# Kernel optimization log

Measured on AMD Instinct MI355X. Metric: run time of the kernel, lower is better.

The kernel has to match this reference:

```python
import jax, jax.numpy as jnp
import numpy as np

MARGIN = 1.0


def setup_inputs() -> dict:
    key = jax.random.key(0)
    k1, k2 = jax.random.split(key)
    N, D = 8192, 128
    embeddings = jax.random.normal(k1, (N, D), dtype=jnp.float32)
    labels = jax.random.randint(k2, (N,), 0, 100, dtype=jnp.int64)
    return {"embeddings": embeddings, "labels": labels}


def reference(embeddings, labels):
    N = embeddings.shape[0]
    # Pairwise Euclidean distances (torch.cdist p=2) via the expanded form.
    sq = jnp.sum(embeddings * embeddings, axis=-1)  # [N]
    d2 = sq[:, None] + sq[None, :] - 2.0 * (embeddings @ embeddings.T)  # [N, N]
    d2 = jnp.maximum(d2, 0.0)
    eye = jnp.eye(N, dtype=bool)
    # Diagonal distances are never used (masked out below); replace the zero
    # under the sqrt to keep gradients finite.
    dist = jnp.sqrt(jnp.where(eye, 1.0, d2))  # [N, N]

    same = labels[:, None] == labels[None, :]
    pos_mask = same & ~eye
    neg_mask = (~same) & ~eye

    # sum_exp_i depends only on row i: one masked row reduction, reused for all pairs.
    sum_exp = jnp.sum(jnp.where(neg_mask, jnp.exp(MARGIN - dist), 0.0), axis=1)  # [N]

    # L_ij = log(sum_exp_i + sum_exp_j) + d_ij, only on positive pairs.
    L = jnp.log(sum_exp[:, None] + sum_exp[None, :]) + dist  # [N, N]
    per_pair = jnp.where(pos_mask, jax.nn.relu(L) ** 2, 0.0)
    n_pos = jnp.sum(pos_mask).astype(per_pair.dtype)
    return jnp.sum(per_pair) / n_pos / 2.0
```

## Files before the change

### kernel.cpp

```cpp
#include <hip/hip_runtime.h>
#include <hip/hip_bf16.h>


typedef __attribute__((ext_vector_type(8))) short bf16x8;
typedef __attribute__((ext_vector_type(4))) float f32x4;

__device__ __forceinline__ unsigned short f2bf(float f) {
    unsigned u = __float_as_uint(f);
    u += 0x7fffu + ((u >> 16) & 1u);
    return (unsigned short)(u >> 16);
}

__global__ __launch_bounds__(256) void setup_kernel(
    const float* __restrict__ e, const int* __restrict__ labels,
    float* __restrict__ sq, unsigned* __restrict__ ebf,
    float* __restrict__ sum_exp,
    int* __restrict__ counts_out, int* __restrict__ offsets_out,
    int* __restrict__ idxbuf, unsigned* __restrict__ ticket, int N)
{
    const int tid = threadIdx.x;
    if ((int)blockIdx.x < (int)gridDim.x - 1) {
        const int lane = tid & 63, wid = tid >> 6;
        if (tid < 32) sum_exp[blockIdx.x * 32 + tid] = 0.f;
        const int rowbase = (blockIdx.x * 4 + wid) * 8;
        #pragma unroll
        for (int it = 0; it < 8; ++it) {
            int row = rowbase + it;
            if (row >= N) break;
            float2 v = ((const float2*)(e + (size_t)row * 128))[lane];
            float s = v.x * v.x + v.y * v.y;
            #pragma unroll
            for (int off = 1; off < 64; off <<= 1) s += __shfl_xor(s, off, 64);
            if (lane == 0) sq[row] = s;
            unsigned bits = (unsigned)f2bf(v.x) | ((unsigned)f2bf(v.y) << 16);
            ebf[(size_t)row * 64 + lane] = bits;
        }
    } else {
        __shared__ int cnt[256];
        __shared__ int off[256];
        if (tid == 0) *ticket = 0u;
        cnt[tid] = 0;
        __syncthreads();
        for (int i = tid; i < N; i += 256)
            atomicAdd(&cnt[(unsigned)labels[i] & 255u], 1);
        __syncthreads();
        if (tid < 64) {
            int base = tid * 4;
            int c0 = cnt[base], c1 = cnt[base+1], c2 = cnt[base+2], c3 = cnt[base+3];
            int s = c0 + c1 + c2 + c3;
            int v = s;
            #pragma unroll
            for (int d = 1; d < 64; d <<= 1) {
                int u = __shfl_up(v, d, 64);
                if (tid >= d) v += u;
            }
            int excl = v - s;
            off[base]     = excl;
            off[base + 1] = excl + c0;
            off[base + 2] = excl + c0 + c1;
            off[base + 3] = excl + c0 + c1 + c2;
        }
        __syncthreads();
        counts_out[tid]  = cnt[tid];
        offsets_out[tid] = off[tid];
        cnt[tid] = off[tid];
        __syncthreads();
        for (int i = tid; i < N; i += 256) {
            int l = (unsigned)labels[i] & 255u;
            int p = atomicAdd(&cnt[l], 1);
            idxbuf[p] = i;
        }
    }
}

__global__ __launch_bounds__(512) void pass1_kernel(
    const unsigned short* __restrict__ ebf,
    const float* __restrict__ sq,
    const int* __restrict__ labels,
    float* __restrict__ sum_exp,
    int N, int nCb)
{
    __shared__ __align__(16) char a_tile[128 * 128];
    __shared__ __align__(16) char b_tile[128 * 128];
    __shared__ float rowsum[128];
    __shared__ float colsum[128];

    const int tid = threadIdx.x;
    const int lane = tid & 63, wid = tid >> 6;

    const int t = blockIdx.x;
    int bi = (int)((2.f * nCb + 1.f - __builtin_amdgcn_sqrtf(
                   (2.f * nCb + 1.f) * (2.f * nCb + 1.f) - 8.f * t)) * 0.5f);
    if (bi < 0) bi = 0;
    if (bi > nCb - 1) bi = nCb - 1;
    while (bi + 1 <= nCb - 1 && (bi + 1) * (2 * nCb - bi) / 2 <= t) ++bi;
    while (bi > 0 && bi * (2 * nCb - bi + 1) / 2 > t) --bi;
    const int bj = bi + (t - bi * (2 * nCb - bi + 1) / 2);
    const bool diag = (bi == bj);
    const int brow = bi * 128, bcol = bj * 128;

    if (tid < 128) { rowsum[tid] = 0.f; colsum[tid] = 0.f; }

    const int wm = (wid >> 2) * 64, wn = (wid & 3) * 32;
    const int lhi = lane >> 4, llo = lane & 15;
    const char* ebfB = (const char*)ebf;

    f32x4 acc[4][2];
    #pragma unroll
    for (int m = 0; m < 4; ++m)
        #pragma unroll
        for (int n = 0; n < 2; ++n)
            acc[m][n] = (f32x4){0.f, 0.f, 0.f, 0.f};

    #pragma unroll
    for (int c = 0; c < 2; ++c) {
        #pragma unroll
        for (int k = 0; k < 4; ++k) {
            int s = wid * 256 + k * 64;
            int tsel = s >> 10;
            int ls = s & 1023;
            int sl = ls + lane;
            int r = sl >> 3, j = sl & 7;
            int grow = (tsel ? bcol : brow) + r;
            const void* g = ebfB + ((size_t)grow << 8) + c * 128 + ((j ^ (r & 7)) << 4);
            char* l = (tsel ? b_tile : a_tile) + ls * 16;
            __builtin_amdgcn_global_load_lds(
                (const __attribute__((address_space(1))) unsigned*)g,
                (__attribute__((address_space(3))) unsigned*)l, 16, 0, 0);
        }
        __syncthreads();

        #pragma unroll
        for (int h = 0; h < 2; ++h) {
            const int cb = h * 64 + lhi * 16;
            bf16x8 af[4], bfr[2];
            #pragma unroll
            for (int m = 0; m < 4; ++m) {
                int r = wm + m * 16 + llo;
                af[m] = *(const bf16x8*)(a_tile + r * 128 + (cb ^ ((r & 7) << 4)));
            }
            #pragma unroll
            for (int n = 0; n < 2; ++n) {
                int r = wn + n * 16 + llo;
                bfr[n] = *(const bf16x8*)(b_tile + r * 128 + (cb ^ ((r & 7) << 4)));
            }
            #pragma unroll
            for (int m = 0; m < 4; ++m)
                #pragma unroll
                for (int n = 0; n < 2; ++n)
                    acc[m][n] = __builtin_amdgcn_mfma_f32_16x16x32_bf16(af[m], bfr[n], acc[m][n], 0, 0, 0);
        }
        __syncthreads();
    }

    const int rowbase = brow + wm;
    float sqr[4][4]; int labr[4][4];
    #pragma unroll
    for (int m = 0; m < 4; ++m)
        #pragma unroll
        for (int r = 0; r < 4; ++r) {
            int row = rowbase + m * 16 + lhi * 4 + r;
            sqr[m][r] = sq[row];
            labr[m][r] = labels[row];
        }
    float sqc[2]; int labc[2];
    #pragma unroll
    for (int n = 0; n < 2; ++n) {
        int col = bcol + wn + n * 16 + llo;
        sqc[n] = sq[col];
        labc[n] = labels[col];
    }

    float wsum[4][4] = {};
    float csum[2] = {};
    #pragma unroll
    for (int m = 0; m < 4; ++m)
        #pragma unroll
        for (int n = 0; n < 2; ++n)
            #pragma unroll
            for (int r = 0; r < 4; ++r) {
                float g = acc[m][n][r];
                float d2 = fmaxf(fmaf(-2.f, g, sqr[m][r] + sqc[n]), 0.f);
                float dist = __builtin_amdgcn_sqrtf(d2);
                float w = (labr[m][r] != labc[n]) ? __expf(-dist) : 0.f;
                wsum[m][r] += w;
                csum[n] += w;
            }
    #pragma unroll
    for (int m = 0; m < 4; ++m)
        #pragma unroll
        for (int r = 0; r < 4; ++r) {
            float s = wsum[m][r];
            #pragma unroll
            for (int off = 1; off < 16; off <<= 1) s += __shfl_xor(s, off, 64);
            if (llo == 0)
                atomicAdd(&rowsum[wm + m * 16 + lhi * 4 + r], s);
        }
    if (!diag) {
        #pragma unroll
        for (int n = 0; n < 2; ++n) {
            float s = csum[n];
            s += __shfl_xor(s, 16, 64);
            s += __shfl_xor(s, 32, 64);
            if (lhi == 0)
                atomicAdd(&colsum[wn + n * 16 + llo], s);
        }
    }
    __syncthreads();
    if (tid < 128) {
        unsafeAtomicAdd(&sum_exp[brow + tid], rowsum[tid]);
        if (!diag)
            unsafeAtomicAdd(&sum_exp[bcol + tid], colsum[tid]);
    }
}

__global__ __launch_bounds__(256) void pass2_kernel(
    const unsigned short* __restrict__ ebf,
    const float* __restrict__ sq,
    const float* __restrict__ sum_exp,
    const int* __restrict__ idxbuf,
    const int* __restrict__ offsets,
    const int* __restrict__ counts,
    double* __restrict__ partial2,
    unsigned* __restrict__ cnt2,
    unsigned* __restrict__ ticket,
    float* __restrict__ out)
{
    __shared__ __align__(16) char a_tile[128 * 128];
    __shared__ __align__(16) char b_tile[128 * 128];
    __shared__ double bsum[4];
    __shared__ unsigned bcnt[4];
    __shared__ bool isLast;

    const int L = blockIdx.x;
    const int NL = gridDim.x;
    const int tid = threadIdx.x;
    const int lane = tid & 63, wid = tid >> 6;
    const int cnt = counts[L], offs = offsets[L];
    const int wm = (wid >> 1) * 64, wn = (wid & 1) * 64;
    const int lhi = lane >> 4, llo = lane & 15;
    const char* ebfB = (const char*)ebf;
    const float E1 = 2.71828182845904523f;

    float lsum = 0.f; unsigned lcnt = 0;

    if (cnt > 1) {
        const int nSub = (cnt + 127) >> 7;
        for (int si = 0; si < nSub; ++si)
        for (int sj = si; sj < nSub; ++sj) {
            const int baseA = offs + si * 128, baseB = offs + sj * 128;
            const int cntA = min(128, cnt - si * 128);
            const int cntB = min(128, cnt - sj * 128);
            const float wgt = (si == sj) ? 1.f : 2.f;
            const unsigned wgtu = (si == sj) ? 1u : 2u;

            f32x4 acc[4][4];
            #pragma unroll
            for (int m = 0; m < 4; ++m)
                #pragma unroll
                for (int n = 0; n < 4; ++n)
                    acc[m][n] = (f32x4){0.f, 0.f, 0.f, 0.f};

            for (int c = 0; c < 2; ++c) {
                #pragma unroll
                for (int i2 = 0; i2 < 8; ++i2) {
                    int sl = tid + i2 * 256;
                    int tsel = sl >> 10;
                    int s = sl & 1023;
                    int r = s >> 3, j = s & 7;
                    int base = tsel ? baseB : baseA;
                    int cc = tsel ? cntB : cntA;
                    int gr = idxbuf[base + min(r, cc - 1)];
                    uint4 v = *(const uint4*)(ebfB + ((size_t)gr << 8) + c * 128 + (j << 4));
                    char* tp = tsel ? b_tile : a_tile;
                    *(uint4*)(tp + r * 128 + (((j << 4)) ^ ((r & 7) << 4))) = v;
                }
                __syncthreads();
                #pragma unroll
                for (int h = 0; h < 2; ++h) {
                    const int cb = h * 64 + lhi * 16;
                    bf16x8 af[4], bfr[4];
                    #pragma unroll
                    for (int m = 0; m < 4; ++m) {
                        int r = wm + m * 16 + llo;
                        af[m] = *(const bf16x8*)(a_tile + r * 128 + (cb ^ ((r & 7) << 4)));
                    }
                    #pragma unroll
                    for (int n = 0; n < 4; ++n) {
                        int r = wn + n * 16 + llo;
                        bfr[n] = *(const bf16x8*)(b_tile + r * 128 + (cb ^ ((r & 7) << 4)));
                    }
                    #pragma unroll
                    for (int m = 0; m < 4; ++m)
                        #pragma unroll
                        for (int n = 0; n < 4; ++n)
                            acc[m][n] = __builtin_amdgcn_mfma_f32_16x16x32_bf16(af[m], bfr[n], acc[m][n], 0, 0, 0);
                }
                __syncthreads();
            }

            int giA[4][4]; float sqA[4][4], seA[4][4]; bool vA[4][4];
            #pragma unroll
            for (int m = 0; m < 4; ++m)
                #pragma unroll
                for (int r = 0; r < 4; ++r) {
                    int lr = wm + m * 16 + lhi * 4 + r;
                    vA[m][r] = lr < cntA;
                    int gi = idxbuf[baseA + min(lr, cntA - 1)];
                    giA[m][r] = gi;
                    sqA[m][r] = sq[gi];
                    seA[m][r] = sum_exp[gi] * E1;
                }
            int gjB[4]; float sqB[4], seB[4]; bool vB[4];
            #pragma unroll
            for (int n = 0; n < 4; ++n) {
                int lc = wn + n * 16 + llo;
                vB[n] = lc < cntB;
                int gj = idxbuf[baseB + min(lc, cntB - 1)];
                gjB[n] = gj;
                sqB[n] = sq[gj];
                seB[n] = sum_exp[gj] * E1;
            }
            #pragma unroll
            for (int m = 0; m < 4; ++m)
                #pragma unroll
                for (int n = 0; n < 4; ++n)
                    #pragma unroll
                    for (int r = 0; r < 4; ++r) {
                        float g = acc[m][n][r];
                        float d2 = fmaxf(fmaf(-2.f, g, sqA[m][r] + sqB[n]), 0.f);
                        float dist = __builtin_amdgcn_sqrtf(d2);
                        bool pos = vA[m][r] && vB[n] && (giA[m][r] != gjB[n]);
                        float Lv = __logf(seA[m][r] + seB[n]) + dist;
                        Lv = fmaxf(Lv, 0.f);
                        lsum += pos ? wgt * Lv * Lv : 0.f;
                        lcnt += pos ? wgtu : 0u;
                    }
        }
    }

    #pragma unroll
    for (int off = 1; off < 64; off <<= 1) {
        lsum += __shfl_xor(lsum, off, 64);
        lcnt += __shfl_xor(lcnt, off, 64);
    }
    if (lane == 0) { bsum[wid] = (double)lsum; bcnt[wid] = lcnt; }
    __syncthreads();
    if (tid == 0) {
        partial2[L] = bsum[0] + bsum[1] + bsum[2] + bsum[3];
        cnt2[L] = bcnt[0] + bcnt[1] + bcnt[2] + bcnt[3];
        __threadfence();
        isLast = (atomicAdd(ticket, 1u) == (unsigned)(NL - 1));
    }
    __syncthreads();

    if (isLast) {
        __threadfence();
        double tt = (tid < NL) ? partial2[tid] : 0.0;
        unsigned c = (tid < NL) ? cnt2[tid] : 0u;
        #pragma unroll
        for (int off = 1; off < 64; off <<= 1) {
            tt += __shfl_xor(tt, off, 64);
            c  += __shfl_xor(c, off, 64);
        }
        if (lane == 0) { bsum[wid] = tt; bcnt[wid] = c; }
        __syncthreads();
        if (tid == 0) {
            double s = bsum[0] + bsum[1] + bsum[2] + bsum[3];
            unsigned cc = bcnt[0] + bcnt[1] + bcnt[2] + bcnt[3];
            if (cc == 0) cc = 1;
            out[0] = (float)(s / (double)cc * 0.5);
        }
    }
}

extern "C" void kernel_launch(void* const* d_in, const int* in_sizes, int n_in,
                              void* d_out, int out_size, void* d_ws, size_t ws_size,
                              hipStream_t stream) {
    const float* e = (const float*)d_in[0];
    const int* labels = (const int*)d_in[1];
    const int N = in_sizes[1];
    const int nCb = N / 128;
    const int nT = nCb * (nCb + 1) / 2;
    const int NL = 256;
    const int nPrep = N / 32;

    char* ws = (char*)d_ws;
    float*    sq       = (float*)ws;
    float*    sum_exp  = (float*)(ws + 4 * (size_t)N);
    unsigned short* ebf = (unsigned short*)(ws + 8 * (size_t)N);
    char*     p        = ws + 8 * (size_t)N + 256 * (size_t)N;
    int*      counts   = (int*)p;      p += NL * 4;
    int*      offsets  = (int*)p;      p += NL * 4;
    unsigned* ticket   = (unsigned*)p; p += 64;
    p = (char*)(((size_t)p + 7) & ~(size_t)7);
    double*   partial2 = (double*)p;   p += NL * 8;
    unsigned* cnt2     = (unsigned*)p; p += NL * 4;
    int*      idxbuf   = (int*)p;

    setup_kernel<<<nPrep + 1, 256, 0, stream>>>(e, labels, sq, (unsigned*)ebf,
                                                sum_exp, counts, offsets,
                                                idxbuf, ticket, N);
    pass1_kernel<<<nT, 512, 0, stream>>>(ebf, sq, labels, sum_exp, N, nCb);
    pass2_kernel<<<NL, 256, 0, stream>>>(ebf, sq, sum_exp, idxbuf, offsets, counts,
                                         partial2, cnt2, ticket, (float*)d_out);
}
```

Before: 72.63 us.

## Process two column tiles per block in pass1, reusing the A strip

Each pass1 block now handles up to two adjacent upper-triangular column tiles for one row block. The full 128x256B A strip is loaded into LDS once and reused, and the B tile loads are split by K-half and pipelined across the tiles. Row sums stay in registers across tiles and the shared-memory rowsum/colsum reductions are replaced with direct global atomics. This halves the grid and cuts redundant A loads, at the cost of less parallelism, more LDS per block and more global atomic traffic.

```diff
diff --git a/kernel.cpp b/kernel.cpp
--- a/kernel.cpp
+++ b/kernel.cpp
@@ -80,50 +80,101 @@
     float* __restrict__ sum_exp,
     int N, int nCb)
 {
-    __shared__ __align__(16) char a_tile[128 * 128];
+    __shared__ __align__(16) char a_tile[128 * 256];
     __shared__ __align__(16) char b_tile[128 * 128];
-    __shared__ float rowsum[128];
-    __shared__ float colsum[128];
 
     const int tid = threadIdx.x;
     const int lane = tid & 63, wid = tid >> 6;
-
-    const int t = blockIdx.x;
-    int bi = (int)((2.f * nCb + 1.f - __builtin_amdgcn_sqrtf(
-                   (2.f * nCb + 1.f) * (2.f * nCb + 1.f) - 8.f * t)) * 0.5f);
-    if (bi < 0) bi = 0;
-    if (bi > nCb - 1) bi = nCb - 1;
-    while (bi + 1 <= nCb - 1 && (bi + 1) * (2 * nCb - bi) / 2 <= t) ++bi;
-    while (bi > 0 && bi * (2 * nCb - bi + 1) / 2 > t) --bi;
-    const int bj = bi + (t - bi * (2 * nCb - bi + 1) / 2);
-    const bool diag = (bi == bj);
-    const int brow = bi * 128, bcol = bj * 128;
-
-    if (tid < 128) { rowsum[tid] = 0.f; colsum[tid] = 0.f; }
-
     const int wm = (wid >> 2) * 64, wn = (wid & 3) * 32;
     const int lhi = lane >> 4, llo = lane & 15;
     const char* ebfB = (const char*)ebf;
 
-    f32x4 acc[4][2];
+    {
+    }
+    int rem = blockIdx.x, bi = 0;
+    while (true) {
+        int c = (nCb - bi + 1) >> 1;
+        if (rem < c) break;
+        rem -= c; ++bi;
+    }
+    const int bj0 = bi + 2 * rem;
+    const int nTiles = min(2, nCb - bj0);
+    const int brow = bi * 128;
+
+    #pragma unroll
+    for (int i = 0; i < 4; ++i) {
+        int sl = tid + i * 512;
+        int r = sl >> 4, j = sl & 15;
+        const void* g = ebfB + ((size_t)(brow + r) << 8) + ((j ^ (r & 7)) << 4);
+        char* l = a_tile + (size_t)(i * 512 + wid * 64) * 16 + lane * 16;
+        __builtin_amdgcn_global_load_lds(
+            (const __attribute__((address_space(1))) unsigned*)g,
+            (__attribute__((address_space(3))) unsigned*)l, 16, 0, 0);
+    }
+    #pragma unroll
+    for (int i = 0; i < 2; ++i) {
+        int sl = tid + i * 512;
+        int r = sl >> 3, j = sl & 7;
+        const void* g = ebfB + ((size_t)(bj0 * 128 + r) << 8) + ((j ^ (r & 7)) << 4);
+        char* l = b_tile + (size_t)(i * 512 + wid * 64) * 16 + lane * 16;
+        __builtin_amdgcn_global_load_lds(
+            (const __attribute__((address_space(1))) unsigned*)g,
+            (__attribute__((address_space(3))) unsigned*)l, 16, 0, 0);
+    }
+    __syncthreads();
+
+    float sqr[4][4]; int labr[4][4];
     #pragma unroll
     for (int m = 0; m < 4; ++m)
         #pragma unroll
-        for (int n = 0; n < 2; ++n)
-            acc[m][n] = (f32x4){0.f, 0.f, 0.f, 0.f};
-
-    #pragma unroll
-    for (int c = 0; c < 2; ++c) {
-        #pragma unroll
-        for (int k = 0; k < 4; ++k) {
-            int s = wid * 256 + k * 64;
-            int tsel = s >> 10;
-            int ls = s & 1023;
-            int sl = ls + lane;
+        for (int r = 0; r < 4; ++r) {
+            int row = brow + wm + m * 16 + lhi * 4 + r;
+            sqr[m][r] = sq[row];
+            labr[m][r] = labels[row];
+        }
+    float wsum[4][4] = {};
+
+    for (int u = 0; u < nTiles; ++u) {
+        const int bj = bj0 + u;
+        const int bcol = bj * 128;
+        const bool diag = (bj == bi);
+
+        f32x4 acc[4][2];
+        #pragma unroll
+        for (int m = 0; m < 4; ++m)
+            #pragma unroll
+            for (int n = 0; n < 2; ++n)
+                acc[m][n] = (f32x4){0.f, 0.f, 0.f, 0.f};
+
+        #pragma unroll
+        for (int h = 0; h < 2; ++h) {
+            const int cba = h * 64 + lhi * 16;
+            const int cbb = h * 64 + lhi * 16;
+            bf16x8 af[4], bfr[2];
+            #pragma unroll
+            for (int m = 0; m < 4; ++m) {
+                int r = wm + m * 16 + llo;
+                af[m] = *(const bf16x8*)(a_tile + r * 256 + (cba ^ ((r & 7) << 4)));
+            }
+            #pragma unroll
+            for (int n = 0; n < 2; ++n) {
+                int r = wn + n * 16 + llo;
+                bfr[n] = *(const bf16x8*)(b_tile + r * 128 + (cbb ^ ((r & 7) << 4)));
+            }
+            #pragma unroll
+            for (int m = 0; m < 4; ++m)
+                #pragma unroll
+                for (int n = 0; n < 2; ++n)
+                    acc[m][n] = __builtin_amdgcn_mfma_f32_16x16x32_bf16(af[m], bfr[n], acc[m][n], 0, 0, 0);
+        }
+        __syncthreads();
+
+        #pragma unroll
+        for (int i = 0; i < 2; ++i) {
+            int sl = tid + i * 512;
             int r = sl >> 3, j = sl & 7;
-            int grow = (tsel ? bcol : brow) + r;
-            const void* g = ebfB + ((size_t)grow << 8) + c * 128 + ((j ^ (r & 7)) << 4);
-            char* l = (tsel ? b_tile : a_tile) + ls * 16;
+            const void* g = ebfB + ((size_t)(bcol + r) << 8) + 128 + ((j ^ (r & 7)) << 4);
+            char* l = b_tile + (size_t)(i * 512 + wid * 64) * 16 + lane * 16;
             __builtin_amdgcn_global_load_lds(
                 (const __attribute__((address_space(1))) unsigned*)g,
                 (__attribute__((address_space(3))) unsigned*)l, 16, 0, 0);
@@ -132,17 +183,18 @@
 
         #pragma unroll
         for (int h = 0; h < 2; ++h) {
-            const int cb = h * 64 + lhi * 16;
+            const int cba = 128 + h * 64 + lhi * 16;
+            const int cbb = h * 64 + lhi * 16;
             bf16x8 af[4], bfr[2];
             #pragma unroll
             for (int m = 0; m < 4; ++m) {
                 int r = wm + m * 16 + llo;
-                af[m] = *(const bf16x8*)(a_tile + r * 128 + (cb ^ ((r & 7) << 4)));
+                af[m] = *(const bf16x8*)(a_tile + r * 256 + (cba ^ ((r & 7) << 4)));
             }
             #pragma unroll
             for (int n = 0; n < 2; ++n) {
                 int r = wn + n * 16 + llo;
-                bfr[n] = *(const bf16x8*)(b_tile + r * 128 + (cb ^ ((r & 7) << 4)));
+                bfr[n] = *(const bf16x8*)(b_tile + r * 128 + (cbb ^ ((r & 7) << 4)));
             }
             #pragma unroll
             for (int m = 0; m < 4; ++m)
@@ -151,67 +203,64 @@
                     acc[m][n] = __builtin_amdgcn_mfma_f32_16x16x32_bf16(af[m], bfr[n], acc[m][n], 0, 0, 0);
         }
         __syncthreads();
-    }
-
-    const int rowbase = brow + wm;
-    float sqr[4][4]; int labr[4][4];
+
+        if (u + 1 < nTiles) {
+            #pragma unroll
+            for (int i = 0; i < 2; ++i) {
+                int sl = tid + i * 512;
+                int r = sl >> 3, j = sl & 7;
+                const void* g = ebfB + ((size_t)(bcol + 128 + r) << 8) + ((j ^ (r & 7)) << 4);
+                char* l = b_tile + (size_t)(i * 512 + wid * 64) * 16 + lane * 16;
+                __builtin_amdgcn_global_load_lds(
+                    (const __attribute__((address_space(1))) unsigned*)g,
+                    (__attribute__((address_space(3))) unsigned*)l, 16, 0, 0);
+            }
+        }
+
+        float sqc[2]; int labc[2];
+        #pragma unroll
+        for (int n = 0; n < 2; ++n) {
+            int col = bcol + wn + n * 16 + llo;
+            sqc[n] = sq[col];
+            labc[n] = labels[col];
+        }
+        float csum[2] = {};
+        #pragma unroll
+        for (int m = 0; m < 4; ++m)
+            #pragma unroll
+            for (int n = 0; n < 2; ++n)
+                #pragma unroll
+                for (int r = 0; r < 4; ++r) {
+                    float g = acc[m][n][r];
+                    float d2 = fmaxf(fmaf(-2.f, g, sqr[m][r] + sqc[n]), 0.f);
+                    float dist = __builtin_amdgcn_sqrtf(d2);
+                    float w = (labr[m][r] != labc[n]) ? __expf(-dist) : 0.f;
+                    wsum[m][r] += w;
+                    csum[n] += w;
+                }
+        if (!diag) {
+            #pragma unroll
+            for (int n = 0; n < 2; ++n) {
+                float s = csum[n];
+                s += __shfl_xor(s, 16, 64);
+                s += __shfl_xor(s, 32, 64);
+                if (lhi == 0)
+                    unsafeAtomicAdd(&sum_exp[bcol + wn + n * 16 + llo], s);
+            }
+        }
+        __syncthreads();
+    }
+
     #pragma unroll
     for (int m = 0; m < 4; ++m)
         #pragma unroll
         for (int r = 0; r < 4; ++r) {
-            int row = rowbase + m * 16 + lhi * 4 + r;
-            sqr[m][r] = sq[row];
-            labr[m][r] = labels[row];
-        }
-    float sqc[2]; int labc[2];
-    #pragma unroll
-    for (int n = 0; n < 2; ++n) {
-        int col = bcol + wn + n * 16 + llo;
-        sqc[n] = sq[col];
-        labc[n] = labels[col];
-    }
-
-    float wsum[4][4] = {};
-    float csum[2] = {};
-    #pragma unroll
-    for (int m = 0; m < 4; ++m)
-        #pragma unroll
-        for (int n = 0; n < 2; ++n)
-            #pragma unroll
-            for (int r = 0; r < 4; ++r) {
-                float g = acc[m][n][r];
-                float d2 = fmaxf(fmaf(-2.f, g, sqr[m][r] + sqc[n]), 0.f);
-                float dist = __builtin_amdgcn_sqrtf(d2);
-                float w = (labr[m][r] != labc[n]) ? __expf(-dist) : 0.f;
-                wsum[m][r] += w;
-                csum[n] += w;
-            }
-    #pragma unroll
-    for (int m = 0; m < 4; ++m)
-        #pragma unroll
-        for (int r = 0; r < 4; ++r) {
             float s = wsum[m][r];
             #pragma unroll
             for (int off = 1; off < 16; off <<= 1) s += __shfl_xor(s, off, 64);
             if (llo == 0)
-                atomicAdd(&rowsum[wm + m * 16 + lhi * 4 + r], s);
-        }
-    if (!diag) {
-        #pragma unroll
-        for (int n = 0; n < 2; ++n) {
-            float s = csum[n];
-            s += __shfl_xor(s, 16, 64);
-            s += __shfl_xor(s, 32, 64);
-            if (lhi == 0)
-                atomicAdd(&colsum[wn + n * 16 + llo], s);
-        }
-    }
-    __syncthreads();
-    if (tid < 128) {
-        unsafeAtomicAdd(&sum_exp[brow + tid], rowsum[tid]);
-        if (!diag)
-            unsafeAtomicAdd(&sum_exp[bcol + tid], colsum[tid]);
-    }
+                unsafeAtomicAdd(&sum_exp[brow + wm + m * 16 + lhi * 4 + r], s);
+        }
 }
 
 __global__ __launch_bounds__(256) void pass2_kernel(
@@ -381,9 +430,11 @@
     const int* labels = (const int*)d_in[1];
     const int N = in_sizes[1];
     const int nCb = N / 128;
-    const int nT = nCb * (nCb + 1) / 2;
     const int NL = 256;
     const int nPrep = N / 32;
+
+    int nStrips = 0;
+    for (int bi = 0; bi < nCb; ++bi) nStrips += (nCb - bi + 1) >> 1;
 
     char* ws = (char*)d_ws;
     float*    sq       = (float*)ws;
@@ -401,7 +452,7 @@
     setup_kernel<<<nPrep + 1, 256, 0, stream>>>(e, labels, sq, (unsigned*)ebf,
                                                 sum_exp, counts, offsets,
                                                 idxbuf, ticket, N);
-    pass1_kernel<<<nT, 512, 0, stream>>>(ebf, sq, labels, sum_exp, N, nCb);
+    pass1_kernel<<<nStrips, 512, 0, stream>>>(ebf, sq, labels, sum_exp, N, nCb);
     pass2_kernel<<<NL, 256, 0, stream>>>(ebf, sq, sum_exp, idxbuf, offsets, counts,
                                          partial2, cnt2, ticket, (float*)d_out);
 }
```

New measurement: 79.36 us. +9.3%, slower.

## Replace sum_exp atomics with per-tile partials and prescale embeddings for exp2

Applied to the files above, without the earlier changes.

Pass1 now writes per-block-column partial row sums to a [nCb x N] buffer instead of atomically adding into sum_exp. Pass2 reduces those partials per label into LDS before its main loop. Embeddings are prescaled by log2(e) so pass1 can use a native exp2 instead of expf, and pass2 multiplies the distance by ln2 to undo the scaling. This removes global float atomics and their zero-init, at the cost of an extra N*nCb float buffer, a serial reduction over nCb in pass2, and a cap of 1024 entries per label in LDS.

```diff
diff --git a/kernel.cpp b/kernel.cpp
--- a/kernel.cpp
+++ b/kernel.cpp
@@ -4,6 +4,12 @@
 
 typedef __attribute__((ext_vector_type(8))) short bf16x8;
 typedef __attribute__((ext_vector_type(4))) float f32x4;
+
+#if __has_builtin(__builtin_amdgcn_exp2f)
+#define EXP2F __builtin_amdgcn_exp2f
+#else
+#define EXP2F exp2f
+#endif
 
 __device__ __forceinline__ unsigned short f2bf(float f) {
     unsigned u = __float_as_uint(f);
@@ -14,20 +20,20 @@
 __global__ __launch_bounds__(256) void setup_kernel(
     const float* __restrict__ e, const int* __restrict__ labels,
     float* __restrict__ sq, unsigned* __restrict__ ebf,
-    float* __restrict__ sum_exp,
     int* __restrict__ counts_out, int* __restrict__ offsets_out,
     int* __restrict__ idxbuf, unsigned* __restrict__ ticket, int N)
 {
     const int tid = threadIdx.x;
+    const float LOG2E = 1.44269504088896341f;
     if ((int)blockIdx.x < (int)gridDim.x - 1) {
         const int lane = tid & 63, wid = tid >> 6;
-        if (tid < 32) sum_exp[blockIdx.x * 32 + tid] = 0.f;
         const int rowbase = (blockIdx.x * 4 + wid) * 8;
         #pragma unroll
         for (int it = 0; it < 8; ++it) {
             int row = rowbase + it;
             if (row >= N) break;
             float2 v = ((const float2*)(e + (size_t)row * 128))[lane];
+            v.x *= LOG2E; v.y *= LOG2E;
             float s = v.x * v.x + v.y * v.y;
             #pragma unroll
             for (int off = 1; off < 64; off <<= 1) s += __shfl_xor(s, off, 64);
@@ -77,7 +83,7 @@
     const unsigned short* __restrict__ ebf,
     const float* __restrict__ sq,
     const int* __restrict__ labels,
-    float* __restrict__ sum_exp,
+    float* __restrict__ partial1,
     int N, int nCb)
 {
     __shared__ __align__(16) char a_tile[128 * 128];
@@ -182,7 +188,7 @@
                 float g = acc[m][n][r];
                 float d2 = fmaxf(fmaf(-2.f, g, sqr[m][r] + sqc[n]), 0.f);
                 float dist = __builtin_amdgcn_sqrtf(d2);
-                float w = (labr[m][r] != labc[n]) ? __expf(-dist) : 0.f;
+                float w = (labr[m][r] != labc[n]) ? EXP2F(0.f - dist) : 0.f;
                 wsum[m][r] += w;
                 csum[n] += w;
             }
@@ -208,26 +214,28 @@
     }
     __syncthreads();
     if (tid < 128) {
-        unsafeAtomicAdd(&sum_exp[brow + tid], rowsum[tid]);
+        partial1[(size_t)bj * N + brow + tid] = rowsum[tid];
         if (!diag)
-            unsafeAtomicAdd(&sum_exp[bcol + tid], colsum[tid]);
+            partial1[(size_t)bi * N + bcol + tid] = colsum[tid];
     }
 }
 
 __global__ __launch_bounds__(256) void pass2_kernel(
     const unsigned short* __restrict__ ebf,
     const float* __restrict__ sq,
-    const float* __restrict__ sum_exp,
+    const float* __restrict__ partial1,
     const int* __restrict__ idxbuf,
     const int* __restrict__ offsets,
     const int* __restrict__ counts,
     double* __restrict__ partial2,
     unsigned* __restrict__ cnt2,
     unsigned* __restrict__ ticket,
-    float* __restrict__ out)
+    float* __restrict__ out,
+    int N, int nCb)
 {
     __shared__ __align__(16) char a_tile[128 * 128];
     __shared__ __align__(16) char b_tile[128 * 128];
+    __shared__ float se_lds[1024];
     __shared__ double bsum[4];
     __shared__ unsigned bcnt[4];
     __shared__ bool isLast;
@@ -241,6 +249,16 @@
     const int lhi = lane >> 4, llo = lane & 15;
     const char* ebfB = (const char*)ebf;
     const float E1 = 2.71828182845904523f;
+    const float LN2 = 0.69314718055994531f;
+
+    const int cnt_c = min(cnt, 1024);
+    for (int i = tid; i < cnt_c; i += 256) {
+        int gi = idxbuf[offs + i];
+        float s = 0.f;
+        for (int cb = 0; cb < nCb; ++cb) s += partial1[(size_t)cb * N + gi];
+        se_lds[i] = s * E1;
+    }
+    __syncthreads();
 
     float lsum = 0.f; unsigned lcnt = 0;
 
@@ -306,20 +324,22 @@
                 for (int r = 0; r < 4; ++r) {
                     int lr = wm + m * 16 + lhi * 4 + r;
                     vA[m][r] = lr < cntA;
+                    int li = min(si * 128 + min(lr, cntA - 1), 1023);
                     int gi = idxbuf[baseA + min(lr, cntA - 1)];
                     giA[m][r] = gi;
                     sqA[m][r] = sq[gi];
-                    seA[m][r] = sum_exp[gi] * E1;
+                    seA[m][r] = se_lds[li];
                 }
             int gjB[4]; float sqB[4], seB[4]; bool vB[4];
             #pragma unroll
             for (int n = 0; n < 4; ++n) {
                 int lc = wn + n * 16 + llo;
                 vB[n] = lc < cntB;
+                int lj = min(sj * 128 + min(lc, cntB - 1), 1023);
                 int gj = idxbuf[baseB + min(lc, cntB - 1)];
                 gjB[n] = gj;
                 sqB[n] = sq[gj];
-                seB[n] = sum_exp[gj] * E1;
+                seB[n] = se_lds[lj];
             }
             #pragma unroll
             for (int m = 0; m < 4; ++m)
@@ -329,7 +349,7 @@
                     for (int r = 0; r < 4; ++r) {
                         float g = acc[m][n][r];
                         float d2 = fmaxf(fmaf(-2.f, g, sqA[m][r] + sqB[n]), 0.f);
-                        float dist = __builtin_amdgcn_sqrtf(d2);
+                        float dist = __builtin_amdgcn_sqrtf(d2) * LN2;
                         bool pos = vA[m][r] && vB[n] && (giA[m][r] != gjB[n]);
                         float Lv = __logf(seA[m][r] + seB[n]) + dist;
                         Lv = fmaxf(Lv, 0.f);
@@ -387,9 +407,10 @@
 
     char* ws = (char*)d_ws;
     float*    sq       = (float*)ws;
-    float*    sum_exp  = (float*)(ws + 4 * (size_t)N);
-    unsigned short* ebf = (unsigned short*)(ws + 8 * (size_t)N);
-    char*     p        = ws + 8 * (size_t)N + 256 * (size_t)N;
+    unsigned short* ebf = (unsigned short*)(ws + 4 * (size_t)N);
+    char*     p        = ws + 4 * (size_t)N + 256 * (size_t)N;
+    float*    partial1 = (float*)p;
+    p += (size_t)nCb * N * 4;
     int*      counts   = (int*)p;      p += NL * 4;
     int*      offsets  = (int*)p;      p += NL * 4;
     unsigned* ticket   = (unsigned*)p; p += 64;
@@ -399,9 +420,8 @@
     int*      idxbuf   = (int*)p;
 
     setup_kernel<<<nPrep + 1, 256, 0, stream>>>(e, labels, sq, (unsigned*)ebf,
-                                                sum_exp, counts, offsets,
-                                                idxbuf, ticket, N);
-    pass1_kernel<<<nT, 512, 0, stream>>>(ebf, sq, labels, sum_exp, N, nCb);
-    pass2_kernel<<<NL, 256, 0, stream>>>(ebf, sq, sum_exp, idxbuf, offsets, counts,
-                                         partial2, cnt2, ticket, (float*)d_out);
+                                                counts, offsets, idxbuf, ticket, N);
+    pass1_kernel<<<nT, 512, 0, stream>>>(ebf, sq, labels, partial1, N, nCb);
+    pass2_kernel<<<NL, 256, 0, stream>>>(ebf, sq, partial1, idxbuf, offsets, counts,
+                                         partial2, cnt2, ticket, (float*)d_out, N, nCb);
 }
```

Measured after the change: 92.98 us. 28.0% more time.
